# Kernel optimization log

Measured on AMD Instinct MI355X. Metric: run time of the kernel, lower is better.

## Reference

```python
import jax, jax.numpy as jnp
import numpy as np

H, W = 5, 11          # fixed spatial map from ConvLSTM2D((5,11), ...)
P = H * W             # 55 pixels; 1x1 convs are per-pixel linear layers
HC = 64               # hidden channels
IC = 2                # input channels
FC_DIMS = [2 * HC * P, 3400, 1000, 500, 50]  # 7040 -> 3400 -> 1000 -> 500 -> 50


def setup_inputs() -> dict:
    key = jax.random.key(0)
    ks = jax.random.split(key, 24)
    B, T = 32, 256
    s = 0.05
    d = {}
    d["x1"] = jax.random.normal(ks[0], (B, T, IC, H, W), jnp.float32)
    d["x2"] = jax.random.normal(ks[1], (B, T, IC, H, W), jnp.float32)
    # ConvLSTM cell params: 1x1 convs fused into (in, 4*HC) matrices, gate order i,f,o,g
    d["wx1"] = jax.random.normal(ks[2], (IC, 4 * HC), jnp.float32) * s
    d["wh1"] = jax.random.normal(ks[3], (HC, 4 * HC), jnp.float32) * s
    d["bx1"] = jax.random.normal(ks[4], (4 * HC,), jnp.float32) * s
    d["bh1"] = jax.random.normal(ks[5], (4 * HC,), jnp.float32) * s
    d["wx2"] = jax.random.normal(ks[6], (IC, 4 * HC), jnp.float32) * s
    d["wh2"] = jax.random.normal(ks[7], (HC, 4 * HC), jnp.float32) * s
    d["bx2"] = jax.random.normal(ks[8], (4 * HC,), jnp.float32) * s
    d["bh2"] = jax.random.normal(ks[9], (4 * HC,), jnp.float32) * s
    # FC stack (stored as (in,out) so y = x @ W + b, equivalent to torch Linear)
    for i in range(4):
        fan_in, fan_out = FC_DIMS[i], FC_DIMS[i + 1]
        lim = 1.0 / np.sqrt(fan_in)
        d[f"fw{i+2}"] = jax.random.uniform(ks[10 + 2 * i], (fan_in, fan_out), jnp.float32, -lim, lim)
        d[f"fb{i+2}"] = jax.random.uniform(ks[11 + 2 * i], (fan_out,), jnp.float32, -lim, lim)
    return d


def _cell_step(h, c, gx, wh, bh):
    # gx: (B,P,4*HC) precomputed x contribution; h,c: (B,P,HC)
    g = gx + h @ wh + bh
    i, f, o, gg = jnp.split(g, 4, axis=-1)
    c = jax.nn.sigmoid(f) * c + jax.nn.sigmoid(i) * jnp.tanh(gg)
    h = jax.nn.sigmoid(o) * jnp.tanh(c)
    return h, c


def _sub_forward(x, wx1, wh1, bx1, bh1, wx2, wh2, bx2, bh2,
                 fw2, fb2, fw3, fb3, fw4, fb4, fw5, fb5):
    B, T = x.shape[0], x.shape[1]
    # (B,T,C,H,W) -> (B,T,P,C): pixels become a batch dim for the 1x1 convs
    xs = x.transpose(0, 1, 3, 4, 2).reshape(B, T, P, IC)
    # Precompute all input-to-gate projections once (big batched GEMM)
    gx1 = jnp.einsum('btpc,cd->btpd', xs, wx1) + bx1            # cell1: forward in time
    gx2 = jnp.einsum('btpc,cd->btpd', xs[:, ::-1], wx2) + bx2   # cell2: reversed in time
    h0 = jnp.zeros((B, P, HC), x.dtype)

    def step(carry, g):
        h1, c1, h2, c2 = carry
        g1, g2 = g
        h1, c1 = _cell_step(h1, c1, g1, wh1, bh1)
        h2, c2 = _cell_step(h2, c2, g2, wh2, bh2)
        return (h1, c1, h2, c2), None

    (h1, _, h2, _), _ = jax.lax.scan(
        step, (h0, h0, h0, h0),
        (gx1.transpose(1, 0, 2, 3), gx2.transpose(1, 0, 2, 3)))

    # torch.cat((h1,h2),1) on (B,HC,H,W) then flatten -> channel-major layout
    out = jnp.concatenate([h1.transpose(0, 2, 1), h2.transpose(0, 2, 1)], axis=1).reshape(B, -1)
    out = out @ fw2 + fb2
    out = out @ fw3 + fb3
    out = out @ fw4 + fb4
    out = out @ fw5 + fb5
    return out


def reference(x1, x2, wx1, wh1, bx1, bh1, wx2, wh2, bx2, bh2,
              fw2, fb2, fw3, fb3, fw4, fb4, fw5, fb5):
    args = (wx1, wh1, bx1, bh1, wx2, wh2, bx2, bh2,
            fw2, fb2, fw3, fb3, fw4, fb4, fw5, fb5)
    out1 = _sub_forward(x1, *args)
    out2 = _sub_forward(x2, *args)
    return (out1, out2)
```

## Files before the change

### kernel.cpp

```cpp
#include <hip/hip_runtime.h>


#define T_STEPS 256
#define PIX 55
#define MT 16
#define TILES 110
#define LSTM_BLOCKS 440
#define INIT_BLOCKS 10
#define LOG2E 1.4426950408889634f
#define FC_SUB 128
#define FC_GRP 16

typedef float f32x4 __attribute__((ext_vector_type(4)));
typedef __bf16 bf16x8 __attribute__((ext_vector_type(8)));
typedef __bf16 bf16x4 __attribute__((ext_vector_type(4)));

__global__ __launch_bounds__(256) void lstm_kernel(
    const float* __restrict__ x1, const float* __restrict__ x2,
    const float* __restrict__ wx1, const float* __restrict__ wh1,
    const float* __restrict__ bx1, const float* __restrict__ bh1,
    const float* __restrict__ wx2, const float* __restrict__ wh2,
    const float* __restrict__ bx2, const float* __restrict__ bh2,
    float* __restrict__ feat,
    const float* __restrict__ fb2, const float* __restrict__ fb3,
    const float* __restrict__ fb4, const float* __restrict__ fb5,
    float* __restrict__ t1, float* __restrict__ t2,
    float* __restrict__ t3, float* __restrict__ o)
{
    int bid  = blockIdx.x;
    int tid  = threadIdx.x;

    if (bid >= LSTM_BLOCKS) {
        int base = (bid - LSTM_BLOCKS) * 256 + tid;
        const int n1 = 64 * 3400, n2 = 64 * 1000, n3 = 64 * 500, n4 = 64 * 50;
        const int tot = n1 + n2 + n3 + n4;
        for (int i = base; i < tot; i += 256 * INIT_BLOCKS) {
            int j = i;
            if (j < n1) { t1[j] = fb2[j % 3400]; continue; }
            j -= n1;
            if (j < n2) { t2[j] = fb3[j % 1000]; continue; }
            j -= n2;
            if (j < n3) { t3[j] = fb4[j % 500]; continue; }
            o[j - n3] = fb5[(j - n3) % 50];
        }
        return;
    }

    int tile = bid % TILES;
    int cc   = bid / TILES;
    int sub  = cc >> 1, cell = cc & 1;
    const float* x  = sub  ? x2  : x1;
    const float* wx = cell ? wx2 : wx1;
    const float* wh = cell ? wh2 : wh1;
    const float* bx = cell ? bx2 : bx1;
    const float* bh = cell ? bh2 : bh1;

    int w    = tid >> 6;
    int l    = tid & 63;
    int quad = l >> 4;
    int c16  = l & 15;

    __shared__ float xl[MT * 514];
    __shared__ __align__(16) __bf16 hb[2][2][MT][72];

    {
        int seq0 = tile * MT;
        for (int i = 0; i < 32; ++i) {
            int idx = tid + 256 * i;
            int m = idx >> 9;
            int tc = idx & 511;
            int t = tc >> 1, c = tc & 1;
            int seq = seq0 + m;
            int b = seq / PIX, p = seq % PIX;
            xl[m * 514 + tc] = x[((b * T_STEPS + t) * 2 + c) * PIX + p];
        }
    }
    {
        __bf16* hz = &hb[0][0][0][0];
        for (int i = tid; i < 2 * 2 * MT * 72; i += 256) hz[i] = (__bf16)0.0f;
    }

    bf16x8 Whi[4][2], Wlo[4][2];
    float btot[4][4], wxa[4][4], wxb[4][4];
#pragma unroll
    for (int g = 0; g < 4; ++g) {
        float sg = (g == 3) ? (-2.0f * LOG2E) : (-LOG2E);
        int col = 64 * g + 16 * w + c16;
#pragma unroll
        for (int r = 0; r < 4; ++r) {
            int u = 64 * g + 16 * w + 4 * quad + r;
            btot[g][r] = sg * (bx[u] + bh[u]);
            wxa[g][r]  = sg * wx[u];
            wxb[g][r]  = sg * wx[256 + u];
        }
#pragma unroll
        for (int q = 0; q < 2; ++q) {
#pragma unroll
            for (int j = 0; j < 8; ++j) {
                int k = 32 * q + 8 * quad + j;
                float wv = sg * wh[k * 256 + col];
                __bf16 hi = (__bf16)wv;
                Whi[g][q][j] = hi;
                Wlo[g][q][j] = (__bf16)(wv - (float)hi);
            }
        }
    }

    float cst[4]  = {0.f, 0.f, 0.f, 0.f};
    float hfin[4] = {0.f, 0.f, 0.f, 0.f};

    __syncthreads();
    float2 xv = *(const float2*)&xl[c16 * 514 + (cell ? (T_STEPS - 1) : 0) * 2];

#pragma unroll 2
    for (int t = 0; t < T_STEPS; ++t) {
        int rb = t & 1, wb = rb ^ 1;

        bf16x8 Bh[2], Bl[2];
#pragma unroll
        for (int q = 0; q < 2; ++q) {
            Bh[q] = *(const bf16x8*)&hb[rb][0][c16][32 * q + 8 * quad];
            Bl[q] = *(const bf16x8*)&hb[rb][1][c16][32 * q + 8 * quad];
        }

        f32x4 acc[4];
#pragma unroll
        for (int g = 0; g < 4; ++g) {
#pragma unroll
            for (int r = 0; r < 4; ++r)
                acc[g][r] = fmaf(xv.y, wxb[g][r], fmaf(xv.x, wxa[g][r], btot[g][r]));
        }
#pragma unroll
        for (int g = 0; g < 4; ++g)
            acc[g] = __builtin_amdgcn_mfma_f32_16x16x32_bf16(Whi[g][0], Bh[0], acc[g], 0, 0, 0);
#pragma unroll
        for (int g = 0; g < 4; ++g)
            acc[g] = __builtin_amdgcn_mfma_f32_16x16x32_bf16(Whi[g][1], Bh[1], acc[g], 0, 0, 0);
#pragma unroll
        for (int g = 0; g < 4; ++g)
            acc[g] = __builtin_amdgcn_mfma_f32_16x16x32_bf16(Wlo[g][0], Bh[0], acc[g], 0, 0, 0);
#pragma unroll
        for (int g = 0; g < 4; ++g)
            acc[g] = __builtin_amdgcn_mfma_f32_16x16x32_bf16(Wlo[g][1], Bh[1], acc[g], 0, 0, 0);
#pragma unroll
        for (int g = 0; g < 4; ++g)
            acc[g] = __builtin_amdgcn_mfma_f32_16x16x32_bf16(Whi[g][0], Bl[0], acc[g], 0, 0, 0);
#pragma unroll
        for (int g = 0; g < 4; ++g)
            acc[g] = __builtin_amdgcn_mfma_f32_16x16x32_bf16(Whi[g][1], Bl[1], acc[g], 0, 0, 0);

        float ei[4], ef[4], eo[4], eg[4];
#pragma unroll
        for (int r = 0; r < 4; ++r) {
            ei[r] = __builtin_amdgcn_exp2f(acc[0][r]);
            ef[r] = __builtin_amdgcn_exp2f(acc[1][r]);
            eo[r] = __builtin_amdgcn_exp2f(acc[2][r]);
            eg[r] = __builtin_amdgcn_exp2f(acc[3][r]);
        }

        bf16x4 ph, pl;
#pragma unroll
        for (int r = 0; r < 4; ++r) {
            float sf  = __builtin_amdgcn_rcpf(1.0f + ef[r]);
            float itg = (1.0f - eg[r]) * __builtin_amdgcn_rcpf((1.0f + ei[r]) * (1.0f + eg[r]));
            float c   = fmaf(sf, cst[r], itg);
            cst[r] = c;
            float ec = __builtin_amdgcn_exp2f(-2.0f * LOG2E * c);
            float h  = (1.0f - ec) * __builtin_amdgcn_rcpf((1.0f + eo[r]) * (1.0f + ec));
            hfin[r] = h;
            __bf16 hi = (__bf16)h;
            ph[r] = hi;
            pl[r] = (__bf16)(h - (float)hi);
        }
        *(bf16x4*)&hb[wb][0][c16][16 * w + 4 * quad] = ph;
        *(bf16x4*)&hb[wb][1][c16][16 * w + 4 * quad] = pl;

        {
            int txn = (cell ? (T_STEPS - 2 - t) : (t + 1)) & 255;
            xv = *(const float2*)&xl[c16 * 514 + txn * 2];
        }
        __syncthreads();
    }

    {
        int seq = tile * MT + c16;
        int b = seq / PIX, p = seq % PIX;
#pragma unroll
        for (int r = 0; r < 4; ++r) {
            int u = 16 * w + 4 * quad + r;
            feat[(size_t)(sub * 32 + b) * 7040 + (cell * 64 + u) * PIX + p] = hfin[r];
        }
    }
}

__global__ __launch_bounds__(256) void fc_gemm(const float* __restrict__ A,
                                               const float* __restrict__ W,
                                               float* __restrict__ out,
                                               int K, int N, int kchunk) {
    __shared__ __align__(16) float al[FC_SUB * 68];
    int tid = threadIdx.x;
    int l   = tid & 63;
    int wv  = tid >> 6;
    int k0   = blockIdx.y * kchunk;
    int kend = min(K, k0 + kchunk);

    int n  = blockIdx.x * 64 + l;
    int ne = min(n, N - 1);

    float acc[16];
#pragma unroll
    for (int i = 0; i < 16; ++i) acc[i] = 0.0f;

    for (int ks = k0; ks < kend; ks += FC_SUB) {
        int kcur = min(FC_SUB, kend - ks);
        __syncthreads();
        if (kcur == FC_SUB) {
#pragma unroll
            for (int i = 0; i < 32; ++i) {
                int idx = tid + 256 * i;
                int m = idx >> 7, kc = idx & 127;
                al[kc * 68 + m] = A[(size_t)m * K + ks + kc];
            }
        } else {
#pragma unroll
            for (int i = 0; i < 32; ++i) {
                int idx = tid + 256 * i;
                int m = idx >> 7, kc = idx & 127;
                if (kc < kcur) al[kc * 68 + m] = A[(size_t)m * K + ks + kc];
            }
        }
        __syncthreads();

        const float* wr = W + (size_t)ks * N + ne;
        if (kcur == FC_SUB) {
#pragma unroll
            for (int g8 = 0; g8 < FC_SUB / FC_GRP; ++g8) {
                float wbuf[FC_GRP];
#pragma unroll
                for (int j = 0; j < FC_GRP; ++j)
                    wbuf[j] = wr[(size_t)(g8 * FC_GRP + j) * N];
#pragma unroll
                for (int j = 0; j < FC_GRP; ++j) {
                    const float4* ap = (const float4*)&al[(g8 * FC_GRP + j) * 68 + 16 * wv];
#pragma unroll
                    for (int i = 0; i < 4; ++i) {
                        float4 a = ap[i];
                        acc[4 * i + 0] = fmaf(a.x, wbuf[j], acc[4 * i + 0]);
                        acc[4 * i + 1] = fmaf(a.y, wbuf[j], acc[4 * i + 1]);
                        acc[4 * i + 2] = fmaf(a.z, wbuf[j], acc[4 * i + 2]);
                        acc[4 * i + 3] = fmaf(a.w, wbuf[j], acc[4 * i + 3]);
                    }
                }
            }
        } else {
            int kc0 = 0;
            for (; kc0 + FC_GRP <= kcur; kc0 += FC_GRP) {
                float wbuf[FC_GRP];
#pragma unroll
                for (int j = 0; j < FC_GRP; ++j)
                    wbuf[j] = wr[(size_t)(kc0 + j) * N];
#pragma unroll
                for (int j = 0; j < FC_GRP; ++j) {
                    const float4* ap = (const float4*)&al[(kc0 + j) * 68 + 16 * wv];
#pragma unroll
                    for (int i = 0; i < 4; ++i) {
                        float4 a = ap[i];
                        acc[4 * i + 0] = fmaf(a.x, wbuf[j], acc[4 * i + 0]);
                        acc[4 * i + 1] = fmaf(a.y, wbuf[j], acc[4 * i + 1]);
                        acc[4 * i + 2] = fmaf(a.z, wbuf[j], acc[4 * i + 2]);
                        acc[4 * i + 3] = fmaf(a.w, wbuf[j], acc[4 * i + 3]);
                    }
                }
            }
            for (; kc0 < kcur; ++kc0) {
                float wvv = wr[(size_t)kc0 * N];
                const float4* ap = (const float4*)&al[kc0 * 68 + 16 * wv];
#pragma unroll
                for (int i = 0; i < 4; ++i) {
                    float4 a = ap[i];
                    acc[4 * i + 0] = fmaf(a.x, wvv, acc[4 * i + 0]);
                    acc[4 * i + 1] = fmaf(a.y, wvv, acc[4 * i + 1]);
                    acc[4 * i + 2] = fmaf(a.z, wvv, acc[4 * i + 2]);
                    acc[4 * i + 3] = fmaf(a.w, wvv, acc[4 * i + 3]);
                }
            }
        }
    }

    if (n < N) {
        float* pr = out + n;
#pragma unroll
        for (int i = 0; i < 16; ++i)
            unsafeAtomicAdd(&pr[(size_t)(16 * wv + i) * N], acc[i]);
    }
}

extern "C" void kernel_launch(void* const* d_in, const int* in_sizes, int n_in,
                              void* d_out, int out_size, void* d_ws, size_t ws_size,
                              hipStream_t stream) {
    const float* x1  = (const float*)d_in[0];
    const float* x2  = (const float*)d_in[1];
    const float* wx1 = (const float*)d_in[2];
    const float* wh1 = (const float*)d_in[3];
    const float* bx1 = (const float*)d_in[4];
    const float* bh1 = (const float*)d_in[5];
    const float* wx2 = (const float*)d_in[6];
    const float* wh2 = (const float*)d_in[7];
    const float* bx2 = (const float*)d_in[8];
    const float* bh2 = (const float*)d_in[9];
    const float* fw2 = (const float*)d_in[10];
    const float* fb2 = (const float*)d_in[11];
    const float* fw3 = (const float*)d_in[12];
    const float* fb3 = (const float*)d_in[13];
    const float* fw4 = (const float*)d_in[14];
    const float* fb4 = (const float*)d_in[15];
    const float* fw5 = (const float*)d_in[16];
    const float* fb5 = (const float*)d_in[17];

    char* ws = (char*)d_ws;
    float* feat = (float*)ws;
    float* t1   = feat + (size_t)64 * 7040;
    float* t2   = t1   + (size_t)64 * 3400;
    float* t3   = t2   + (size_t)64 * 1000;
    float* o    = (float*)d_out;

    lstm_kernel<<<dim3(LSTM_BLOCKS + INIT_BLOCKS), dim3(256), 0, stream>>>(
        x1, x2, wx1, wh1, bx1, bh1, wx2, wh2, bx2, bh2, feat,
        fb2, fb3, fb4, fb5, t1, t2, t3, o);

    fc_gemm<<<dim3(54, 28), dim3(256), 0, stream>>>(feat, fw2, t1, 7040, 3400, 256);
    fc_gemm<<<dim3(16, 54), dim3(256), 0, stream>>>(t1, fw3, t2, 3400, 1000, 64);
    fc_gemm<<<dim3(8, 16), dim3(256), 0, stream>>>(t2, fw4, t3, 1000, 500, 64);
    fc_gemm<<<dim3(1, 16), dim3(256), 0, stream>>>(t3, fw5, o, 500, 50, 32);
}
```

Before: 535.9 us.

## Fuse four FC GEMM launches into one persistent kernel with grid barriers

Replaces the four separate fc_gemm launches with one persistent fc_fused kernel of 512 blocks. Each block loops over that layer's work units, and a global atomic-counter barrier separates the layers. The counters are zeroed by the init blocks of the LSTM kernel. This removes three kernel launch gaps and their tail effects, but all 512 blocks must be co-resident or the spin barrier deadlocks, and the late layers leave most blocks idle.

```diff
diff --git a/kernel.cpp b/kernel.cpp
--- a/kernel.cpp
+++ b/kernel.cpp
@@ -10,6 +10,7 @@
 #define LOG2E 1.4426950408889634f
 #define FC_SUB 128
 #define FC_GRP 16
+#define FC_BLOCKS 512
 
 typedef float f32x4 __attribute__((ext_vector_type(4)));
 typedef __bf16 bf16x8 __attribute__((ext_vector_type(8)));
@@ -25,12 +26,14 @@
     const float* __restrict__ fb2, const float* __restrict__ fb3,
     const float* __restrict__ fb4, const float* __restrict__ fb5,
     float* __restrict__ t1, float* __restrict__ t2,
-    float* __restrict__ t3, float* __restrict__ o)
+    float* __restrict__ t3, float* __restrict__ o,
+    int* __restrict__ ctrs)
 {
     int bid  = blockIdx.x;
     int tid  = threadIdx.x;
 
     if (bid >= LSTM_BLOCKS) {
+        if (bid == LSTM_BLOCKS && tid < 3) ctrs[tid] = 0;
         int base = (bid - LSTM_BLOCKS) * 256 + tid;
         const int n1 = 64 * 3400, n2 = 64 * 1000, n3 = 64 * 500, n4 = 64 * 50;
         const int tot = n1 + n2 + n3 + n4;
@@ -193,18 +196,27 @@
     }
 }
 
-__global__ __launch_bounds__(256) void fc_gemm(const float* __restrict__ A,
-                                               const float* __restrict__ W,
-                                               float* __restrict__ out,
-                                               int K, int N, int kchunk) {
-    __shared__ __align__(16) float al[FC_SUB * 68];
-    int tid = threadIdx.x;
-    int l   = tid & 63;
-    int wv  = tid >> 6;
-    int k0   = blockIdx.y * kchunk;
+__device__ __forceinline__ void gbar(int* c, int target) {
+    __syncthreads();
+    if (threadIdx.x == 0) {
+        __threadfence();
+        __hip_atomic_fetch_add(c, 1, __ATOMIC_RELAXED, __HIP_MEMORY_SCOPE_AGENT);
+        while (__hip_atomic_load(c, __ATOMIC_RELAXED, __HIP_MEMORY_SCOPE_AGENT) < target)
+            __builtin_amdgcn_s_sleep(2);
+        __threadfence();
+    }
+    __syncthreads();
+}
+
+__device__ __forceinline__ void fc_unit(const float* __restrict__ A,
+                                        const float* __restrict__ W,
+                                        float* __restrict__ out,
+                                        int K, int N, int kchunk,
+                                        int nx, int ky, float* al,
+                                        int tid, int l, int wv) {
+    int k0   = ky * kchunk;
     int kend = min(K, k0 + kchunk);
-
-    int n  = blockIdx.x * 64 + l;
+    int n  = nx * 64 + l;
     int ne = min(n, N - 1);
 
     float acc[16];
@@ -293,6 +305,32 @@
         for (int i = 0; i < 16; ++i)
             unsafeAtomicAdd(&pr[(size_t)(16 * wv + i) * N], acc[i]);
     }
+}
+
+__global__ __launch_bounds__(256) void fc_fused(
+    const float* __restrict__ feat, const float* __restrict__ fw2, float* __restrict__ t1,
+    const float* __restrict__ fw3, float* __restrict__ t2,
+    const float* __restrict__ fw4, float* __restrict__ t3,
+    const float* __restrict__ fw5, float* __restrict__ o,
+    int* __restrict__ ctrs)
+{
+    __shared__ __align__(16) float al[FC_SUB * 68];
+    int tid = threadIdx.x;
+    int l   = tid & 63;
+    int wv  = tid >> 6;
+    int G   = gridDim.x;
+
+    for (int u = blockIdx.x; u < 54 * 28; u += G)
+        fc_unit(feat, fw2, t1, 7040, 3400, 256, u % 54, u / 54, al, tid, l, wv);
+    gbar(&ctrs[0], G);
+    for (int u = blockIdx.x; u < 16 * 54; u += G)
+        fc_unit(t1, fw3, t2, 3400, 1000, 64, u % 16, u / 16, al, tid, l, wv);
+    gbar(&ctrs[1], G);
+    for (int u = blockIdx.x; u < 8 * 16; u += G)
+        fc_unit(t2, fw4, t3, 1000, 500, 64, u % 8, u / 8, al, tid, l, wv);
+    gbar(&ctrs[2], G);
+    for (int u = blockIdx.x; u < 16; u += G)
+        fc_unit(t3, fw5, o, 500, 50, 32, 0, u, al, tid, l, wv);
 }
 
 extern "C" void kernel_launch(void* const* d_in, const int* in_sizes, int n_in,
@@ -322,14 +360,13 @@
     float* t1   = feat + (size_t)64 * 7040;
     float* t2   = t1   + (size_t)64 * 3400;
     float* t3   = t2   + (size_t)64 * 1000;
+    int*   ctrs = (int*)(t3 + (size_t)64 * 500);
     float* o    = (float*)d_out;
 
     lstm_kernel<<<dim3(LSTM_BLOCKS + INIT_BLOCKS), dim3(256), 0, stream>>>(
         x1, x2, wx1, wh1, bx1, bh1, wx2, wh2, bx2, bh2, feat,
-        fb2, fb3, fb4, fb5, t1, t2, t3, o);
-
-    fc_gemm<<<dim3(54, 28), dim3(256), 0, stream>>>(feat, fw2, t1, 7040, 3400, 256);
-    fc_gemm<<<dim3(16, 54), dim3(256), 0, stream>>>(t1, fw3, t2, 3400, 1000, 64);
-    fc_gemm<<<dim3(8, 16), dim3(256), 0, stream>>>(t2, fw4, t3, 1000, 500, 64);
-    fc_gemm<<<dim3(1, 16), dim3(256), 0, stream>>>(t3, fw5, o, 500, 50, 32);
-}
+        fb2, fb3, fb4, fb5, t1, t2, t3, o, ctrs);
+
+    fc_fused<<<dim3(FC_BLOCKS), dim3(256), 0, stream>>>(
+        feat, fw2, t1, fw3, t2, fw4, t3, fw5, o, ctrs);
+}
```

Result: slower. 690.0 us (+28.8%).

## Remap FC GEMM so lanes own rows and weights load as wave-uniform scalars

Applied to the files above, without the earlier changes.

Restructures the FC GEMM so each lane handles one batch row (m=lane) and each wave handles 16 consecutive output columns. The weight values are then wave-uniform and can be fetched with scalar loads, while the activation comes from shared memory as a single value per k. The K sub-tile shrinks from 128 to 64, and the accumulators are transposed through shared memory before the atomic adds so the global writes stay coalesced. The trade-off is that weight reads now depend on scalar-cache bandwidth, and there is an extra LDS round trip at the end.

```diff
diff --git a/kernel.cpp b/kernel.cpp
--- a/kernel.cpp
+++ b/kernel.cpp
@@ -8,8 +8,6 @@
 #define LSTM_BLOCKS 440
 #define INIT_BLOCKS 10
 #define LOG2E 1.4426950408889634f
-#define FC_SUB 128
-#define FC_GRP 16
 
 typedef float f32x4 __attribute__((ext_vector_type(4)));
 typedef __bf16 bf16x8 __attribute__((ext_vector_type(8)));
@@ -197,101 +195,76 @@
                                                const float* __restrict__ W,
                                                float* __restrict__ out,
                                                int K, int N, int kchunk) {
-    __shared__ __align__(16) float al[FC_SUB * 68];
+    __shared__ float al[64 * 65];
     int tid = threadIdx.x;
     int l   = tid & 63;
-    int wv  = tid >> 6;
+    int wvu = __builtin_amdgcn_readfirstlane(tid >> 6);
+
     int k0   = blockIdx.y * kchunk;
     int kend = min(K, k0 + kchunk);
-
-    int n  = blockIdx.x * 64 + l;
-    int ne = min(n, N - 1);
+    int n0b  = blockIdx.x * 64;
+    int n0   = n0b + 16 * wvu;
+    bool full = (n0 + 16 <= N);
 
     float acc[16];
 #pragma unroll
-    for (int i = 0; i < 16; ++i) acc[i] = 0.0f;
-
-    for (int ks = k0; ks < kend; ks += FC_SUB) {
-        int kcur = min(FC_SUB, kend - ks);
+    for (int j = 0; j < 16; ++j) acc[j] = 0.0f;
+
+    for (int ks = k0; ks < kend; ks += 64) {
+        int kcur = min(64, kend - ks);
         __syncthreads();
-        if (kcur == FC_SUB) {
-#pragma unroll
-            for (int i = 0; i < 32; ++i) {
-                int idx = tid + 256 * i;
-                int m = idx >> 7, kc = idx & 127;
-                al[kc * 68 + m] = A[(size_t)m * K + ks + kc];
-            }
-        } else {
-#pragma unroll
-            for (int i = 0; i < 32; ++i) {
-                int idx = tid + 256 * i;
-                int m = idx >> 7, kc = idx & 127;
-                if (kc < kcur) al[kc * 68 + m] = A[(size_t)m * K + ks + kc];
-            }
+#pragma unroll
+        for (int i = 0; i < 16; ++i) {
+            int idx = tid + 256 * i;
+            int m = idx >> 6, kc = idx & 63;
+            if (kc < kcur) al[kc * 65 + m] = A[(size_t)m * K + ks + kc];
         }
         __syncthreads();
 
-        const float* wr = W + (size_t)ks * N + ne;
-        if (kcur == FC_SUB) {
-#pragma unroll
-            for (int g8 = 0; g8 < FC_SUB / FC_GRP; ++g8) {
-                float wbuf[FC_GRP];
-#pragma unroll
-                for (int j = 0; j < FC_GRP; ++j)
-                    wbuf[j] = wr[(size_t)(g8 * FC_GRP + j) * N];
-#pragma unroll
-                for (int j = 0; j < FC_GRP; ++j) {
-                    const float4* ap = (const float4*)&al[(g8 * FC_GRP + j) * 68 + 16 * wv];
-#pragma unroll
-                    for (int i = 0; i < 4; ++i) {
-                        float4 a = ap[i];
-                        acc[4 * i + 0] = fmaf(a.x, wbuf[j], acc[4 * i + 0]);
-                        acc[4 * i + 1] = fmaf(a.y, wbuf[j], acc[4 * i + 1]);
-                        acc[4 * i + 2] = fmaf(a.z, wbuf[j], acc[4 * i + 2]);
-                        acc[4 * i + 3] = fmaf(a.w, wbuf[j], acc[4 * i + 3]);
-                    }
+        const float* wr = W + (size_t)ks * N + n0;
+        if (full) {
+            if (kcur == 64) {
+#pragma unroll
+                for (int kc = 0; kc < 64; ++kc) {
+                    float a = al[kc * 65 + l];
+#pragma unroll
+                    for (int j = 0; j < 16; ++j)
+                        acc[j] = fmaf(a, wr[(size_t)kc * N + j], acc[j]);
+                }
+            } else {
+                for (int kc = 0; kc < kcur; ++kc) {
+                    float a = al[kc * 65 + l];
+#pragma unroll
+                    for (int j = 0; j < 16; ++j)
+                        acc[j] = fmaf(a, wr[(size_t)kc * N + j], acc[j]);
                 }
             }
         } else {
-            int kc0 = 0;
-            for (; kc0 + FC_GRP <= kcur; kc0 += FC_GRP) {
-                float wbuf[FC_GRP];
-#pragma unroll
-                for (int j = 0; j < FC_GRP; ++j)
-                    wbuf[j] = wr[(size_t)(kc0 + j) * N];
-#pragma unroll
-                for (int j = 0; j < FC_GRP; ++j) {
-                    const float4* ap = (const float4*)&al[(kc0 + j) * 68 + 16 * wv];
-#pragma unroll
-                    for (int i = 0; i < 4; ++i) {
-                        float4 a = ap[i];
-                        acc[4 * i + 0] = fmaf(a.x, wbuf[j], acc[4 * i + 0]);
-                        acc[4 * i + 1] = fmaf(a.y, wbuf[j], acc[4 * i + 1]);
-                        acc[4 * i + 2] = fmaf(a.z, wbuf[j], acc[4 * i + 2]);
-                        acc[4 * i + 3] = fmaf(a.w, wbuf[j], acc[4 * i + 3]);
-                    }
-                }
+            for (int kc = 0; kc < kcur; ++kc) {
+                float a = al[kc * 65 + l];
+#pragma unroll
+                for (int j = 0; j < 16; ++j)
+                    if (n0 + j < N)
+                        acc[j] = fmaf(a, wr[(size_t)kc * N + j], acc[j]);
             }
-            for (; kc0 < kcur; ++kc0) {
-                float wvv = wr[(size_t)kc0 * N];
-                const float4* ap = (const float4*)&al[kc0 * 68 + 16 * wv];
-#pragma unroll
-                for (int i = 0; i < 4; ++i) {
-                    float4 a = ap[i];
-                    acc[4 * i + 0] = fmaf(a.x, wvv, acc[4 * i + 0]);
-                    acc[4 * i + 1] = fmaf(a.y, wvv, acc[4 * i + 1]);
-                    acc[4 * i + 2] = fmaf(a.z, wvv, acc[4 * i + 2]);
-                    acc[4 * i + 3] = fmaf(a.w, wvv, acc[4 * i + 3]);
-                }
+        }
+    }
+
+    __syncthreads();
+#pragma unroll
+    for (int j = 0; j < 16; ++j)
+        al[l * 65 + 16 * wvu + j] = acc[j];
+    __syncthreads();
+    {
+        int nc = l;
+        int n  = n0b + nc;
+        if (n < N) {
+#pragma unroll
+            for (int i = 0; i < 16; ++i) {
+                int m = 16 * wvu + i;
+                unsafeAtomicAdd(&out[(size_t)m * N + n], al[m * 65 + nc]);
             }
         }
-    }
-
-    if (n < N) {
-        float* pr = out + n;
-#pragma unroll
-        for (int i = 0; i < 16; ++i)
-            unsafeAtomicAdd(&pr[(size_t)(16 * wv + i) * N], acc[i]);
     }
 }
 
```

New measurement: 759.4 us. 1.42x slower.
